# Kernel optimization log

Hardware: AMD Instinct MI355X
Metric: run time of the kernel (lower is better)

## Reference

```python
import jax, jax.numpy as jnp
import numpy as np

SIM = 100      # topk k
GCH = SIM + 1  # group size after concat
LCH = 80       # low-rank mid channels
D = 96         # embed dim


def setup_inputs() -> dict:
    key = jax.random.key(0)
    ks = jax.random.split(key, 14)
    b, N, W, p = 1, 4, 16, 128
    def lin(kw, kb, out_f, in_f):
        s = 1.0 / np.sqrt(in_f)
        w = jax.random.uniform(kw, (out_f, in_f), minval=-s, maxval=s, dtype=jnp.float32)
        bb = jax.random.uniform(kb, (out_f,), minval=-s, maxval=s, dtype=jnp.float32)
        return w, bb
    attn = jax.random.normal(ks[0], (b, N, W, 1, p, p), dtype=jnp.float32)
    v = jax.random.normal(ks[1], (b, N, W, 1, p, D), dtype=jnp.float32)
    mb = jax.random.normal(ks[2], (LCH, 1), dtype=jnp.float32)
    w_sub, b_sub = lin(ks[3], ks[4], LCH, GCH)
    w_up, b_up = lin(ks[5], ks[6], GCH, LCH)
    w_q, b_q = lin(ks[7], ks[8], D, D)
    w_k, b_k = lin(ks[9], ks[10], D, D)
    w_o, b_o = lin(ks[11], ks[12], D, D)
    return {"attn": attn, "v": v, "mb": mb, "w_sub": w_sub, "b_sub": b_sub,
            "w_up": w_up, "b_up": b_up, "w_q": w_q, "b_q": b_q,
            "w_k": w_k, "b_k": b_k, "w_o": w_o, "b_o": b_o}


def reference(attn, v, mb, w_sub, b_sub, w_up, b_up, w_q, b_q, w_k, b_k, w_o, b_o):
    b, N, W, _, p, _ = attn.shape
    c = v.shape[-1]
    # topk + scatter(binary mask) + boolean-compact gather == gather v rows at
    # ascending-sorted topk indices (boolean masking preserves index order).
    _, idx = jax.lax.top_k(attn, SIM)            # [b,N,W,1,p,SIM]
    idx = jnp.sort(idx[:, :, :, 0], axis=-1)     # [b,N,W,p,SIM]
    vq = v[:, :, :, 0]                            # [b,N,W,p,c]
    bI = jnp.arange(b)[:, None, None, None, None]
    nI = jnp.arange(N)[None, :, None, None, None]
    wI = jnp.arange(W)[None, None, :, None, None]
    gathered = vq[bI, nI, wI, idx]                # [b,N,W,p,SIM,c]
    group3d = jnp.concatenate([vq[:, :, :, :, None, :], gathered], axis=4)  # [b,N,W,p,GCH,c]
    # ChannelAttention (memory_blocks=1): pool over c, low-rank memory bank
    y = jnp.mean(group3d, axis=-1)                # [b,N,W,p,GCH]
    lr = y @ w_sub.T + b_sub                      # [b,N,W,p,LCH]
    f1 = (lr @ mb) * (LCH ** -0.5)                # [b,N,W,p,1]
    f_dic = jax.nn.softmax(f1[..., None, :], axis=-1)   # [b,N,W,p,1,1] == 1
    y1 = f_dic * mb[:, 0]                         # [b,N,W,p,1,LCH]
    scale = jax.nn.sigmoid(y1 @ w_up.T + b_up)    # [b,N,W,p,1,GCH]
    scale = scale.reshape(b, N, W, p, GCH, 1)     # matches torch .view(b,N,Nwin,p,n,-1)
    g = group3d * scale
    # StructuralSelfAttention (num_heads=1): query = group element 0, keys/values = rest
    x = g[:, :, :, :, :1, :]                      # [b,N,W,p,1,c]
    yk = g[:, :, :, :, 1:, :]                     # [b,N,W,p,SIM,c]
    q = x @ w_q.T + b_q
    k = yk @ w_k.T + b_k
    scores = jnp.einsum('bnwpqc,bnwpkc->bnwpqk', q, k) / jnp.sqrt(jnp.float32(c))
    wgt = jax.nn.softmax(scores, axis=-1)
    out = jnp.einsum('bnwpqk,bnwpkc->bnwpqc', wgt, yk)  # v = y (no v_proj in source)
    out = out.reshape(b, N, W, p, c)
    return out @ w_o.T + b_o
```

## Files before the change

kernel.cpp:

```cpp
#include <hip/hip_runtime.h>
#include <hip/hip_bf16.h>

#define NW 64
#define P 128
#define D 96
#define PD (P*D)
#define GCH 101
#define SIM 100
#define LCH 80
#define RSQRT96 0.10206207261596577f

#define WS_SCALE 0
#define WS_Q     128
#define WS_KT    (128 + 786432)
#define WS_VO    (128 + 2*786432)

typedef unsigned long long ull;

__device__ __forceinline__ ull make_key(float a, int idx) {
  unsigned u = __float_as_uint(a);
  unsigned msk = (u & 0x80000000u) ? 0xFFFFFFFFu : 0x80000000u;
  return (((ull)(u ^ msk)) << 32) | (unsigned)(127 - idx);
}

__global__ __launch_bounds__(128, 2) void proj_kernel(const float* __restrict__ v,
    const float* __restrict__ wq, const float* __restrict__ bq,
    const float* __restrict__ wk, const float* __restrict__ wo,
    const float* __restrict__ mb, const float* __restrict__ w_up,
    const float* __restrict__ b_up, float* __restrict__ ws) {
  int bid = blockIdx.x;
  int xcd = bid & 7;
  int m = bid >> 3;
  int g = m / 12;
  int rem = m - g * 12;
  int nw = (g << 3) | xcd;
  int pj = rem >> 2, rh = rem & 3;
  const float* W = (pj == 0) ? wq : (pj == 1) ? wk : wo;
  __shared__ float sWt[96 * 100];
  __shared__ float sV[32 * 97];
  int t = threadIdx.x;
  int ty = t >> 3;
  int tx = t & 7;

  for (int k = 0; k < 72; ++k) {
    int idx = t + 128 * k;
    int c = idx / 96, d = idx - c * 96;
    sWt[d * 100 + c] = W[idx];
  }
  const float* Vg = v + (size_t)nw * PD + rh * (32 * D);
#pragma unroll
  for (int i = 0; i < 6; ++i) {
    int idx = (t + 128 * i) * 4;
    float4 x = *(const float4*)(Vg + idx);
    int r = idx / 96, d = idx - r * 96;
    float* p = &sV[r * 97 + d];
    p[0] = x.x; p[1] = x.y; p[2] = x.z; p[3] = x.w;
  }
  float scale0 = 0.f;
  if (pj == 0) {
    float a = b_up[0];
    for (int j = 0; j < LCH; ++j) a += w_up[j] * mb[j];
    scale0 = RSQRT96 / (1.f + __expf(-a));
  }
  __syncthreads();

  float acc[2][12];
#pragma unroll
  for (int a = 0; a < 2; ++a)
#pragma unroll
    for (int j = 0; j < 12; ++j) acc[a][j] = 0.f;

  for (int d = 0; d < 96; ++d) {
    float va0 = sV[(ty * 2 + 0) * 97 + d];
    float va1 = sV[(ty * 2 + 1) * 97 + d];
    const float4* wp = (const float4*)&sWt[d * 100 + tx * 12];
    float4 w0 = wp[0], w1 = wp[1], w2 = wp[2];
    float wb[12] = {w0.x,w0.y,w0.z,w0.w, w1.x,w1.y,w1.z,w1.w, w2.x,w2.y,w2.z,w2.w};
#pragma unroll
    for (int j = 0; j < 12; ++j) {
      acc[0][j] += va0 * wb[j];
      acc[1][j] += va1 * wb[j];
    }
  }

  if (pj == 1) {
    float* ktp = ws + WS_KT + nw * PD;
#pragma unroll
    for (int a = 0; a < 2; ++a) {
      int r = rh * 32 + ty * 2 + a;
#pragma unroll
      for (int j = 0; j < 12; ++j)
        ktp[(tx * 12 + j) * P + r] = acc[a][j];
    }
  } else {
    float* outp = ws + ((pj == 0) ? WS_Q : WS_VO) + nw * PD + (rh * 32) * D;
    float4 bq4[3];
    if (pj == 0) {
      const float4* bp = (const float4*)(bq + tx * 12);
      bq4[0] = bp[0]; bq4[1] = bp[1]; bq4[2] = bp[2];
#pragma unroll
      for (int q = 0; q < 3; ++q) {
        bq4[q].x *= RSQRT96; bq4[q].y *= RSQRT96;
        bq4[q].z *= RSQRT96; bq4[q].w *= RSQRT96;
      }
    }
#pragma unroll
    for (int a = 0; a < 2; ++a) {
      float* orow = outp + (ty * 2 + a) * D + tx * 12;
#pragma unroll
      for (int q = 0; q < 3; ++q) {
        float4 o;
        o.x = acc[a][4*q+0]; o.y = acc[a][4*q+1];
        o.z = acc[a][4*q+2]; o.w = acc[a][4*q+3];
        if (pj == 0) {
          o.x = scale0 * o.x + bq4[q].x; o.y = scale0 * o.y + bq4[q].y;
          o.z = scale0 * o.z + bq4[q].z; o.w = scale0 * o.w + bq4[q].w;
        }
        *(float4*)(orow + 4 * q) = o;
      }
    }
  }

  if (bid == 0 && t < GCH) {
    float a = b_up[t];
    for (int j = 0; j < LCH; ++j) a += w_up[t * LCH + j] * mb[j];
    ws[WS_SCALE + t] = 1.f / (1.f + __expf(-a));
  }
}

__global__ __launch_bounds__(256, 2) void attn_kernel(const float* __restrict__ attn,
    const float* __restrict__ bo, const float* __restrict__ ws,
    float* __restrict__ out) {
  int bid = blockIdx.x;
  int xcd = bid & 7;
  int k = (bid >> 3) & 15;
  int g = bid >> 7;
  int nw = (g << 3) | xcd;
  int wvu = __builtin_amdgcn_readfirstlane(threadIdx.x >> 6);
  int lane = threadIdx.x & 63;
  int p0 = (k * 4 + wvu) * 2;
  __shared__ float sT[4][2][128];

  const float* Kt  = ws + WS_KT + nw * PD;
  const float* VO  = ws + WS_VO + nw * PD;
  const float* Qb  = ws + WS_Q  + nw * PD + p0 * D;
  const float* Ab  = attn + (size_t)(nw * P + p0) * P;
  const float* scl = ws + WS_SCALE;

  ull ke[2], ko[2];
#pragma unroll
  for (int r = 0; r < 2; ++r) {
    float2 a2 = ((const float2*)(Ab + r * P))[lane];
    ke[r] = make_key(a2.x, 2 * lane);
    ko[r] = make_key(a2.y, 2 * lane + 1);
  }

  int ce[2] = {0, 0}, co_[2] = {0, 0};
  for (int jb = 0; jb < P; jb += 8) {
    float aj[2][8];
#pragma unroll
    for (int r = 0; r < 2; ++r)
#pragma unroll
      for (int i = 0; i < 8; ++i) aj[r][i] = Ab[r * P + jb + i];
#pragma unroll
    for (int i = 0; i < 8; ++i) {
      int j = jb + i;
#pragma unroll
      for (int r = 0; r < 2; ++r) {
        ull kj = make_key(aj[r][i], j);
        ce[r]  += (kj > ke[r]) ? 1 : 0;
        co_[r] += (kj > ko[r]) ? 1 : 0;
      }
    }
  }

  float se[2] = {0, 0}, so[2] = {0, 0};
  for (int cb = 0; cb < D; cb += 8) {
    float q[2][8];
#pragma unroll
    for (int r = 0; r < 2; ++r)
#pragma unroll
      for (int i = 0; i < 8; ++i) q[r][i] = Qb[r * D + cb + i];
#pragma unroll
    for (int i = 0; i < 8; ++i) {
      float2 kv = ((const float2*)(Kt + (cb + i) * P))[lane];
#pragma unroll
      for (int r = 0; r < 2; ++r) {
        se[r] += q[r][i] * kv.x;
        so[r] += q[r][i] * kv.y;
      }
    }
  }

  ull lm = (1ull << lane) - 1ull;
#pragma unroll
  for (int r = 0; r < 2; ++r) {
    bool kpe = ce[r] < SIM, kpo = co_[r] < SIM;
    ull be = __ballot(kpe), bo_ = __ballot(kpo);
    int pe = __popcll(be & lm) + __popcll(bo_ & lm);
    int po = pe + (kpe ? 1 : 0);
    float sve = kpe ? scl[1 + pe] : 0.f;
    float svo = kpo ? scl[1 + po] : 0.f;
    float xe = kpe ? sve * se[r] : -1e30f;
    float xo = kpo ? svo * so[r] : -1e30f;
    float mx = fmaxf(xe, xo);
#pragma unroll
    for (int off = 1; off < 64; off <<= 1) mx = fmaxf(mx, __shfl_xor(mx, off));
    float ee = kpe ? __expf(xe - mx) : 0.f;
    float eo = kpo ? __expf(xo - mx) : 0.f;
    float s = ee + eo;
#pragma unroll
    for (int off = 1; off < 64; off <<= 1) s += __shfl_xor(s, off);
    float inv = 1.f / s;
    float2 tw; tw.x = ee * inv * sve; tw.y = eo * inv * svo;
    ((float2*)sT[wvu][r])[lane] = tw;
  }

  int lc = (lane < 48) ? lane : 47;
  float2 o0 = {0.f, 0.f}, o1 = {0.f, 0.f};
#pragma unroll 2
  for (int jb = 0; jb < P; jb += 4) {
    float4 t0 = *(const float4*)&sT[wvu][0][jb];
    float4 t1 = *(const float4*)&sT[wvu][1][jb];
    float tb0[4] = {t0.x, t0.y, t0.z, t0.w};
    float tb1[4] = {t1.x, t1.y, t1.z, t1.w};
#pragma unroll
    for (int jj = 0; jj < 4; ++jj) {
      float2 vo = ((const float2*)(VO + (jb + jj) * D))[lc];
      o0.x += tb0[jj] * vo.x; o0.y += tb0[jj] * vo.y;
      o1.x += tb1[jj] * vo.x; o1.y += tb1[jj] * vo.y;
    }
  }
  if (lane < 48) {
    float2 bb = ((const float2*)bo)[lane];
    float* op = out + (size_t)(nw * P + p0) * D;
    float2 r0; r0.x = o0.x + bb.x; r0.y = o0.y + bb.y;
    float2 r1; r1.x = o1.x + bb.x; r1.y = o1.y + bb.y;
    ((float2*)(op + 0 * D))[lane] = r0;
    ((float2*)(op + 1 * D))[lane] = r1;
  }
}

extern "C" void kernel_launch(void* const* d_in, const int* in_sizes, int n_in,
                              void* d_out, int out_size, void* d_ws, size_t ws_size,
                              hipStream_t stream) {
  const float* attn = (const float*)d_in[0];
  const float* v    = (const float*)d_in[1];
  const float* mb   = (const float*)d_in[2];
  const float* w_up = (const float*)d_in[5];
  const float* b_up = (const float*)d_in[6];
  const float* w_q  = (const float*)d_in[7];
  const float* b_q  = (const float*)d_in[8];
  const float* w_k  = (const float*)d_in[9];
  const float* w_o  = (const float*)d_in[11];
  const float* b_o  = (const float*)d_in[12];
  float* out = (float*)d_out;
  float* ws = (float*)d_ws;

  hipLaunchKernelGGL(proj_kernel, dim3(768), dim3(128), 0, stream,
                     v, w_q, b_q, w_k, w_o, mb, w_up, b_up, ws);
  hipLaunchKernelGGL(attn_kernel, dim3(1024), dim3(256), 0, stream,
                     attn, b_o, ws, out);
}
```

Measured before the change: 65.42 us.

## Rank via wave readlane instead of global reloads; batch loads in attn loops

The top-k rank computation no longer reloads each attention row element from global memory. It broadcasts the already-loaded per-lane ordered keys across the wave with readlane, fully unrolled over 128 positions. The QK and weighted-VO loops are restructured to issue 16 global loads up front before the FMAs, which increases memory-level parallelism. The cost is higher register pressure and a larger code size from the full unroll.

```diff
diff --git a/kernel.cpp b/kernel.cpp
--- a/kernel.cpp
+++ b/kernel.cpp
@@ -17,10 +17,10 @@
 
 typedef unsigned long long ull;
 
-__device__ __forceinline__ ull make_key(float a, int idx) {
+__device__ __forceinline__ unsigned ord_u32(float a) {
   unsigned u = __float_as_uint(a);
   unsigned msk = (u & 0x80000000u) ? 0xFFFFFFFFu : 0x80000000u;
-  return (((ull)(u ^ msk)) << 32) | (unsigned)(127 - idx);
+  return u ^ msk;
 }
 
 __global__ __launch_bounds__(128, 2) void proj_kernel(const float* __restrict__ v,
@@ -147,48 +147,51 @@
   const float* Ab  = attn + (size_t)(nw * P + p0) * P;
   const float* scl = ws + WS_SCALE;
 
+  unsigned he[2], ho[2];
   ull ke[2], ko[2];
 #pragma unroll
   for (int r = 0; r < 2; ++r) {
     float2 a2 = ((const float2*)(Ab + r * P))[lane];
-    ke[r] = make_key(a2.x, 2 * lane);
-    ko[r] = make_key(a2.y, 2 * lane + 1);
+    unsigned ue = ord_u32(a2.x), uo = ord_u32(a2.y);
+    he[r] = ue; ho[r] = uo;
+    ke[r] = (((ull)ue) << 32) | (unsigned)(127 - 2 * lane);
+    ko[r] = (((ull)uo) << 32) | (unsigned)(127 - (2 * lane + 1));
   }
 
   int ce[2] = {0, 0}, co_[2] = {0, 0};
-  for (int jb = 0; jb < P; jb += 8) {
-    float aj[2][8];
-#pragma unroll
-    for (int r = 0; r < 2; ++r)
-#pragma unroll
-      for (int i = 0; i < 8; ++i) aj[r][i] = Ab[r * P + jb + i];
-#pragma unroll
-    for (int i = 0; i < 8; ++i) {
-      int j = jb + i;
-#pragma unroll
-      for (int r = 0; r < 2; ++r) {
-        ull kj = make_key(aj[r][i], j);
-        ce[r]  += (kj > ke[r]) ? 1 : 0;
-        co_[r] += (kj > ko[r]) ? 1 : 0;
-      }
-    }
+#pragma unroll
+  for (int j = 0; j < 128; ++j) {
+    unsigned lo = (unsigned)(127 - j);
+    unsigned h0, h1;
+    if ((j & 1) == 0) {
+      h0 = (unsigned)__builtin_amdgcn_readlane((int)he[0], j >> 1);
+      h1 = (unsigned)__builtin_amdgcn_readlane((int)he[1], j >> 1);
+    } else {
+      h0 = (unsigned)__builtin_amdgcn_readlane((int)ho[0], j >> 1);
+      h1 = (unsigned)__builtin_amdgcn_readlane((int)ho[1], j >> 1);
+    }
+    ull kj0 = (((ull)h0) << 32) | lo;
+    ull kj1 = (((ull)h1) << 32) | lo;
+    ce[0]  += (kj0 > ke[0]) ? 1 : 0;
+    co_[0] += (kj0 > ko[0]) ? 1 : 0;
+    ce[1]  += (kj1 > ke[1]) ? 1 : 0;
+    co_[1] += (kj1 > ko[1]) ? 1 : 0;
   }
 
   float se[2] = {0, 0}, so[2] = {0, 0};
-  for (int cb = 0; cb < D; cb += 8) {
-    float q[2][8];
-#pragma unroll
-    for (int r = 0; r < 2; ++r)
-#pragma unroll
-      for (int i = 0; i < 8; ++i) q[r][i] = Qb[r * D + cb + i];
-#pragma unroll
-    for (int i = 0; i < 8; ++i) {
-      float2 kv = ((const float2*)(Kt + (cb + i) * P))[lane];
-#pragma unroll
-      for (int r = 0; r < 2; ++r) {
-        se[r] += q[r][i] * kv.x;
-        so[r] += q[r][i] * kv.y;
-      }
+#pragma unroll 1
+  for (int cb = 0; cb < D; cb += 16) {
+    float2 kv[16];
+#pragma unroll
+    for (int i = 0; i < 16; ++i)
+      kv[i] = ((const float2*)(Kt + (cb + i) * P))[lane];
+    float q0[16], q1[16];
+#pragma unroll
+    for (int i = 0; i < 16; ++i) { q0[i] = Qb[cb + i]; q1[i] = Qb[D + cb + i]; }
+#pragma unroll
+    for (int i = 0; i < 16; ++i) {
+      se[0] += q0[i] * kv[i].x; so[0] += q0[i] * kv[i].y;
+      se[1] += q1[i] * kv[i].x; so[1] += q1[i] * kv[i].y;
     }
   }
 
@@ -218,17 +221,28 @@
 
   int lc = (lane < 48) ? lane : 47;
   float2 o0 = {0.f, 0.f}, o1 = {0.f, 0.f};
-#pragma unroll 2
-  for (int jb = 0; jb < P; jb += 4) {
-    float4 t0 = *(const float4*)&sT[wvu][0][jb];
-    float4 t1 = *(const float4*)&sT[wvu][1][jb];
-    float tb0[4] = {t0.x, t0.y, t0.z, t0.w};
-    float tb1[4] = {t1.x, t1.y, t1.z, t1.w};
-#pragma unroll
-    for (int jj = 0; jj < 4; ++jj) {
-      float2 vo = ((const float2*)(VO + (jb + jj) * D))[lc];
-      o0.x += tb0[jj] * vo.x; o0.y += tb0[jj] * vo.y;
-      o1.x += tb1[jj] * vo.x; o1.y += tb1[jj] * vo.y;
+#pragma unroll 1
+  for (int jb = 0; jb < P; jb += 16) {
+    float2 vo[16];
+#pragma unroll
+    for (int i = 0; i < 16; ++i)
+      vo[i] = ((const float2*)(VO + (jb + i) * D))[lc];
+    float4 t0v[4], t1v[4];
+#pragma unroll
+    for (int q = 0; q < 4; ++q) {
+      t0v[q] = *(const float4*)&sT[wvu][0][jb + 4 * q];
+      t1v[q] = *(const float4*)&sT[wvu][1][jb + 4 * q];
+    }
+#pragma unroll
+    for (int q = 0; q < 4; ++q) {
+      float ta[4] = {t0v[q].x, t0v[q].y, t0v[q].z, t0v[q].w};
+      float tb[4] = {t1v[q].x, t1v[q].y, t1v[q].z, t1v[q].w};
+#pragma unroll
+      for (int jj = 0; jj < 4; ++jj) {
+        float2 vv = vo[4 * q + jj];
+        o0.x += ta[jj] * vv.x; o0.y += ta[jj] * vv.y;
+        o1.x += tb[jj] * vv.x; o1.y += tb[jj] * vv.y;
+      }
     }
   }
   if (lane < 48) {
```

After: 58.46 us. 1.12x faster.
